# Kernel optimization log

Hardware: AMD Instinct MI355X
Metric: run time of the kernel (lower is better)

The kernel has to match this reference:

```python
import jax, jax.numpy as jnp
import numpy as np

NUM_HEADS = 16

def setup_inputs() -> dict:
    key = jax.random.key(0)
    ks = jax.random.split(key, 5)
    B, T, C = 2, 2048, 1024
    s = 0.02
    return {
        "x": jax.random.normal(ks[0], (B, T, C), dtype=jnp.float32),
        "in_w": jax.random.normal(ks[1], (3 * C, C), dtype=jnp.float32) * s,
        "in_b": jax.random.normal(ks[2], (3 * C,), dtype=jnp.float32) * s,
        "out_w": jax.random.normal(ks[3], (C, C), dtype=jnp.float32) * s,
        "out_b": jax.random.normal(ks[4], (C,), dtype=jnp.float32) * s,
    }

def reference(x, in_w, in_b, out_w, out_b):
    B, T, C = x.shape
    H = NUM_HEADS
    D = C // H
    qvk = x @ in_w.T + in_b  # (B, T, 3C)
    # einops 'b t (d k h) -> k b h t d': factor 3C as (D, 3, H), D outermost
    qvk = qvk.reshape(B, T, D, 3, H).transpose(3, 0, 4, 1, 2)  # (3, B, H, T, D)
    q, v, k = qvk[0], qvk[1], qvk[2]  # note q, v, k assignment order
    scores = jnp.einsum('bhid,bhjd->bhij', q, k) * (D ** -0.5)  # (B, H, T, T)
    causal = jnp.tril(jnp.ones((T, T), dtype=bool))
    scores = jnp.where(causal, scores, -jnp.inf)
    attn = jax.nn.softmax(scores, axis=-1)
    out = jnp.einsum('bhij,bhjd->bhid', attn, v)  # (B, H, T, D)
    out = out.transpose(0, 2, 1, 3).reshape(B, T, C)  # 'b h t d -> b t (h d)'
    return out @ out_w.T + out_b
```

## Files before the change

kernel.cpp:

```cpp
#include <hip/hip_runtime.h>


#define BB 2
#define TT 2048
#define CC 1024
#define HH 16
#define DD 64
#define MM (BB*TT)
#define N3 (3*CC)
#define BH (BB*HH)
#define KSCALE 0.18033688011112042f

typedef unsigned short u16;
typedef unsigned int   u32;
typedef __bf16 bf16x8 __attribute__((ext_vector_type(8)));
typedef float  f32x4  __attribute__((ext_vector_type(4)));

__device__ __forceinline__ u16 f32_to_bf16(float f) {
  u32 u = __float_as_uint(f);
  return (u16)((u + 0x7fffu + ((u >> 16) & 1u)) >> 16);
}
__device__ __forceinline__ u32 pack2_bf16(float a, float b) {
  u32 ua = __float_as_uint(a) + 0x8000u;
  u32 ub = __float_as_uint(b) + 0x8000u;
  return __builtin_amdgcn_perm(ub, ua, 0x07060302);
}

#define N4_X  (MM * CC / 4)
#define N4_W  (N3 * CC / 4)
#define N4_OW (CC * CC / 4)
__global__ __launch_bounds__(256) void cast_all(const float* __restrict__ x,
                                                const float* __restrict__ in_w,
                                                const float* __restrict__ out_w,
                                                u16* __restrict__ xb,
                                                u16* __restrict__ wb,
                                                u16* __restrict__ owb) {
  int i = blockIdx.x * 256 + threadIdx.x;
  const float* src; u16* dst; int j; int sj;
  if (i < N4_X)             { src = x;     dst = xb;  j = i;               sj = j; }
  else if (i < N4_X + N4_W) { src = in_w;  dst = wb;  j = i - N4_X;
                              int rp = j >> 8, c = j & 255;
                              int s = rp >> 10, h = (rp >> 6) & 15, d = rp & 63;
                              sj = (d * 48 + s * 16 + h) * 256 + c; }
  else                      { src = out_w; dst = owb; j = i - N4_X - N4_W; sj = j; }
  float4 f = reinterpret_cast<const float4*>(src)[sj];
  uint2 pk;
  pk.x = (u32)f32_to_bf16(f.x) | ((u32)f32_to_bf16(f.y) << 16);
  pk.y = (u32)f32_to_bf16(f.z) | ((u32)f32_to_bf16(f.w) << 16);
  reinterpret_cast<uint2*>(dst)[j] = pk;
}

__device__ __forceinline__ void gemm_core(const u16* __restrict__ Ag,
                                          const u16* __restrict__ Bg,
                                          int K, u16* Al, u16* Bl,
                                          int m0, int n0, f32x4 acc[4][4]) {
  const int tid = threadIdx.x, lane = tid & 63, w = tid >> 6;
  const int quad = lane >> 4, colr = lane & 15;
  const int mw = (w >> 1) * 64, nw = (w & 1) * 64;
  const int srow = lane >> 3, scol = lane & 7;
  const uint4* Al4 = reinterpret_cast<const uint4*>(Al);
  const uint4* Bl4 = reinterpret_cast<const uint4*>(Bl);
  for (int kt = 0; kt < K / 64; ++kt) {
    __syncthreads();
    #pragma unroll
    for (int ii = 0; ii < 4; ++ii) {
      int inst = w * 4 + ii;
      int row = inst * 8 + srow;
      int cs = scol ^ (row & 7);
      const u16* ga = Ag + (size_t)(m0 + row) * K + kt * 64 + cs * 8;
      const u16* gb = Bg + (size_t)(n0 + row) * K + kt * 64 + cs * 8;
      __builtin_amdgcn_global_load_lds(
          (const __attribute__((address_space(1))) void*)ga,
          (__attribute__((address_space(3))) void*)(Al + inst * 512), 16, 0, 0);
      __builtin_amdgcn_global_load_lds(
          (const __attribute__((address_space(1))) void*)gb,
          (__attribute__((address_space(3))) void*)(Bl + inst * 512), 16, 0, 0);
    }
    __syncthreads();
    #pragma unroll
    for (int ks = 0; ks < 2; ++ks) {
      bf16x8 af[4], bfr[4];
      #pragma unroll
      for (int t = 0; t < 4; ++t) {
        int mrow = mw + t * 16 + colr;
        af[t]  = __builtin_bit_cast(bf16x8, Al4[mrow * 8 + ((ks * 4 + quad) ^ (mrow & 7))]);
        int nrow = nw + t * 16 + colr;
        bfr[t] = __builtin_bit_cast(bf16x8, Bl4[nrow * 8 + ((ks * 4 + quad) ^ (nrow & 7))]);
      }
      #pragma unroll
      for (int mt = 0; mt < 4; ++mt)
        #pragma unroll
        for (int nt = 0; nt < 4; ++nt)
          acc[mt][nt] = __builtin_amdgcn_mfma_f32_16x16x32_bf16(af[mt], bfr[nt], acc[mt][nt], 0, 0, 0);
    }
  }
}

__global__ __launch_bounds__(256) void gemm_qkv(const u16* __restrict__ xb,
                                                const u16* __restrict__ wb,
                                                const float* __restrict__ in_b,
                                                u16* __restrict__ qkv) {
  __shared__ __align__(16) u16 Al[128 * 64];
  __shared__ __align__(16) u16 Bl[128 * 64];
  const int lane = threadIdx.x & 63, w = threadIdx.x >> 6;
  const int quad = lane >> 4, colr = lane & 15;
  const int mw = (w >> 1) * 64, nw = (w & 1) * 64;
  const int m0 = blockIdx.x * 128, n0 = blockIdx.y * 128;
  f32x4 acc[4][4];
  #pragma unroll
  for (int mt = 0; mt < 4; ++mt)
    #pragma unroll
    for (int nt = 0; nt < 4; ++nt) acc[mt][nt] = (f32x4){0.f, 0.f, 0.f, 0.f};
  gemm_core(xb, wb, CC, Al, Bl, m0, n0, acc);
  const int b_ = m0 >> 11;
  #pragma unroll
  for (int nt = 0; nt < 4; ++nt) {
    int np = n0 + nw + nt * 16 + colr;
    int s = np >> 10, h = (np >> 6) & 15, d = np & 63;
    float bias = in_b[d * 48 + s * 16 + h];
    float sc = (s == 2) ? KSCALE : 1.0f;
    u16* base = qkv + ((size_t)(s * BH + b_ * HH + h) * TT) * DD + d;
    #pragma unroll
    for (int mt = 0; mt < 4; ++mt)
      #pragma unroll
      for (int e = 0; e < 4; ++e) {
        int t = (m0 + mw + mt * 16 + quad * 4 + e) & (TT - 1);
        base[(size_t)t * DD] = f32_to_bf16((acc[mt][nt][e] + bias) * sc);
      }
  }
}

__global__ __launch_bounds__(128, 2) void attn_mfma(const u16* __restrict__ qkv,
                                                    u16* __restrict__ aout,
                                                    float* __restrict__ po,
                                                    float* __restrict__ pl) {
  __shared__ __align__(16) u32 Vt[2][64 * 36];
  __shared__ __align__(16) u32 Pl[2 * 32 * 36];
  const int tid  = threadIdx.x;
  const int lane = tid & 63, w = tid >> 6;
  const int quad = lane >> 4, colr = lane & 15;
  const int f = blockIdx.x;
  const int hf = (f >> 3) & 1;
  const int pr = (f >> 4) & 15;
  const int bh = (f & 7) * 4 + (f >> 8);
  const int b_ = bh >> 4, h = bh & 15;
  const int slot = (((bh << 4) + pr) << 1) | hf;

  const uint4* Qg4 = reinterpret_cast<const uint4*>(qkv + (size_t)bh * TT * DD);
  const uint4* Vg4 = reinterpret_cast<const uint4*>(qkv + ((size_t)BH + bh) * TT * DD);
  const uint4* Kg4 = reinterpret_cast<const uint4*>(qkv + ((size_t)2 * BH + bh) * TT * DD);
  const uint4* Pl4 = reinterpret_cast<const uint4*>(Pl);

  const int s_jp = tid & 31, s_half = tid >> 5;
  const int wb32 = w * (32 * 36);

  const int nseg = 2 - hf;
  for (int sg = 0; sg < nseg; ++sg) {
    const bool final_out = (hf == 0) && (sg == 0);
    const int qt  = final_out ? pr : (31 - pr);
    const int jlo = (hf == 1) ? (16 - pr) : 0;
    const int jhi = (hf == 1) ? (31 - pr) : (sg == 0 ? pr : 15 - pr);
    const int i0 = qt * 64;

    bf16x8 qa[2][2];
    #pragma unroll
    for (int u = 0; u < 2; ++u)
      #pragma unroll
      for (int ks = 0; ks < 2; ++ks)
        qa[u][ks] = __builtin_bit_cast(bf16x8,
            Qg4[(size_t)(i0 + w * 32 + u * 16 + colr) * 8 + ks * 4 + quad]);

    f32x4 oacc[2][4];
    #pragma unroll
    for (int u = 0; u < 2; ++u)
      #pragma unroll
      for (int dt = 0; dt < 4; ++dt) oacc[u][dt] = (f32x4){0.f, 0.f, 0.f, 0.f};
    float lp[2] = {0.f, 0.f};

    uint4 va[2], vb[2];
    #pragma unroll
    for (int io = 0; io < 2; ++io) {
      va[io] = Vg4[(size_t)(jlo * 64 + 2 * s_jp) * 8 + s_half + io * 4];
      vb[io] = Vg4[(size_t)(jlo * 64 + 2 * s_jp + 1) * 8 + s_half + io * 4];
    }

    for (int jt = jlo; jt <= jhi; ++jt) {
      const int j0 = jt * 64;
      u32* vtw = Vt[jt & 1];
      const uint4* vt4 = reinterpret_cast<const uint4*>(Vt[jt & 1]);

      #pragma unroll
      for (int io = 0; io < 2; ++io) {
        const int oc = s_half + io * 4;
        u32 aw[4] = {va[io].x, va[io].y, va[io].z, va[io].w};
        u32 bw[4] = {vb[io].x, vb[io].y, vb[io].z, vb[io].w};
        #pragma unroll
        for (int m = 0; m < 4; ++m) {
          vtw[(oc * 8 + 2 * m)     * 36 + s_jp] = __builtin_amdgcn_perm(bw[m], aw[m], 0x05040100);
          vtw[(oc * 8 + 2 * m + 1) * 36 + s_jp] = __builtin_amdgcn_perm(bw[m], aw[m], 0x07060302);
        }
      }
      if (jt < jhi) {
        int nj = j0 + 64;
        #pragma unroll
        for (int io = 0; io < 2; ++io) {
          va[io] = Vg4[(size_t)(nj + 2 * s_jp) * 8 + s_half + io * 4];
          vb[io] = Vg4[(size_t)(nj + 2 * s_jp + 1) * 8 + s_half + io * 4];
        }
      }
      __syncthreads();

      f32x4 sacc[2][4];
      #pragma unroll
      for (int u = 0; u < 2; ++u)
        #pragma unroll
        for (int t4 = 0; t4 < 4; ++t4) sacc[u][t4] = (f32x4){0.f, 0.f, 0.f, 0.f};
      #pragma unroll
      for (int ks = 0; ks < 2; ++ks) {
        uint4 kk[4];
        #pragma unroll
        for (int t4 = 0; t4 < 4; ++t4)
          kk[t4] = Kg4[(size_t)(j0 + t4 * 16 + colr) * 8 + ks * 4 + quad];
        #pragma unroll
        for (int t4 = 0; t4 < 4; ++t4) {
          bf16x8 kb = __builtin_bit_cast(bf16x8, kk[t4]);
          #pragma unroll
          for (int u = 0; u < 2; ++u)
            sacc[u][t4] = __builtin_amdgcn_mfma_f32_16x16x32_bf16(kb, qa[u][ks], sacc[u][t4], 0, 0, 0);
        }
      }

      if (jt == qt) {
        #pragma unroll
        for (int u = 0; u < 2; ++u) {
          const int qv = w * 32 + u * 16 + colr;
          #pragma unroll
          for (int t4 = 0; t4 < 4; ++t4) {
            float p0 = __builtin_amdgcn_exp2f(sacc[u][t4][0]);
            float p1 = __builtin_amdgcn_exp2f(sacc[u][t4][1]);
            float p2 = __builtin_amdgcn_exp2f(sacc[u][t4][2]);
            float p3 = __builtin_amdgcn_exp2f(sacc[u][t4][3]);
            int jb = t4 * 16 + quad * 4;
            if (jb + 0 > qv) p0 = 0.f;
            if (jb + 1 > qv) p1 = 0.f;
            if (jb + 2 > qv) p2 = 0.f;
            if (jb + 3 > qv) p3 = 0.f;
            lp[u] += (p0 + p1) + (p2 + p3);
            uint2 pw; pw.x = pack2_bf16(p0, p1); pw.y = pack2_bf16(p2, p3);
            *reinterpret_cast<uint2*>(Pl + wb32 + (u * 16 + colr) * 36 + t4 * 8 + quad * 2) = pw;
          }
        }
      } else {
        #pragma unroll
        for (int u = 0; u < 2; ++u)
          #pragma unroll
          for (int t4 = 0; t4 < 4; ++t4) {
            float p0 = __builtin_amdgcn_exp2f(sacc[u][t4][0]);
            float p1 = __builtin_amdgcn_exp2f(sacc[u][t4][1]);
            float p2 = __builtin_amdgcn_exp2f(sacc[u][t4][2]);
            float p3 = __builtin_amdgcn_exp2f(sacc[u][t4][3]);
            lp[u] += (p0 + p1) + (p2 + p3);
            uint2 pw; pw.x = pack2_bf16(p0, p1); pw.y = pack2_bf16(p2, p3);
            *reinterpret_cast<uint2*>(Pl + wb32 + (u * 16 + colr) * 36 + t4 * 8 + quad * 2) = pw;
          }
      }

      #pragma unroll
      for (int u = 0; u < 2; ++u) {
        bf16x8 pa[2];
        #pragma unroll
        for (int ks = 0; ks < 2; ++ks)
          pa[ks] = __builtin_bit_cast(bf16x8,
              Pl4[(wb32 + (u * 16 + colr) * 36 + ks * 16 + quad * 4) >> 2]);
        #pragma unroll
        for (int dt = 0; dt < 4; ++dt)
          #pragma unroll
          for (int ks = 0; ks < 2; ++ks) {
            bf16x8 vfr = __builtin_bit_cast(bf16x8, vt4[(dt * 16 + colr) * 9 + ks * 4 + quad]);
            oacc[u][dt] = __builtin_amdgcn_mfma_f32_16x16x32_bf16(pa[ks], vfr, oacc[u][dt], 0, 0, 0);
          }
      }
    }

    #pragma unroll
    for (int u = 0; u < 2; ++u) {
      float ls = lp[u];
      ls += __shfl_xor(ls, 16);
      ls += __shfl_xor(ls, 32);
      if (final_out) {
        float linv[4];
        #pragma unroll
        for (int rg = 0; rg < 4; ++rg)
          linv[rg] = 1.0f / __shfl(ls, quad * 4 + rg);
        #pragma unroll
        for (int dt = 0; dt < 4; ++dt)
          #pragma unroll
          for (int rg = 0; rg < 4; ++rg) {
            int ig = i0 + w * 32 + u * 16 + quad * 4 + rg;
            size_t off = ((size_t)(b_ * TT + ig)) * CC + h * DD + dt * 16 + colr;
            aout[off] = (u16)((__float_as_uint(oacc[u][dt][rg] * linv[rg]) + 0x8000u) >> 16);
          }
      } else {
        float* ob = po + (size_t)slot * 4096;
        #pragma unroll
        for (int dt = 0; dt < 4; ++dt)
          #pragma unroll
          for (int rg = 0; rg < 4; ++rg)
            ob[(w * 32 + u * 16 + quad * 4 + rg) * 64 + dt * 16 + colr] = oacc[u][dt][rg];
        if (quad == 0) pl[slot * 64 + w * 32 + u * 16 + colr] = ls;
      }
    }
    __syncthreads();
  }
}

__global__ __launch_bounds__(256) void attn_finalize(const float* __restrict__ po,
                                                     const float* __restrict__ pl,
                                                     u16* __restrict__ ab) {
  const int blk = blockIdx.x;
  const int bh = blk >> 4, pr = blk & 15;
  const int qt = 31 - pr;
  const int b_ = bh >> 4, h = bh & 15;
  const int t = threadIdx.x;
  const int r = t >> 2, dq = t & 3;
  const size_t s0 = (size_t)blk * 2, s1 = s0 + 1;
  const float4* o0 = reinterpret_cast<const float4*>(po + s0 * 4096 + r * 64 + dq * 16);
  const float4* o1 = reinterpret_cast<const float4*>(po + s1 * 4096 + r * 64 + dq * 16);
  float inv = 1.0f / (pl[s0 * 64 + r] + pl[s1 * 64 + r]);
  u16* dst = ab + ((size_t)(b_ * TT + qt * 64 + r)) * CC + h * DD + dq * 16;
  #pragma unroll
  for (int c = 0; c < 4; ++c) {
    float4 a = o0[c], b = o1[c];
    uint2 pk;
    pk.x = pack2_bf16((a.x + b.x) * inv, (a.y + b.y) * inv);
    pk.y = pack2_bf16((a.z + b.z) * inv, (a.w + b.w) * inv);
    *reinterpret_cast<uint2*>(dst + c * 4) = pk;
  }
}

__global__ __launch_bounds__(256) void gemm_out(const u16* __restrict__ ab,
                                                const u16* __restrict__ owb,
                                                const float* __restrict__ out_b,
                                                float* __restrict__ out) {
  __shared__ __align__(16) u16 Al[128 * 64];
  __shared__ __align__(16) u16 Bl[128 * 64];
  const int lane = threadIdx.x & 63, w = threadIdx.x >> 6;
  const int quad = lane >> 4, colr = lane & 15;
  const int mw = (w >> 1) * 64, nw = (w & 1) * 64;
  const int m0 = blockIdx.x * 128, n0 = blockIdx.y * 128;
  f32x4 acc[4][4];
  #pragma unroll
  for (int mt = 0; mt < 4; ++mt)
    #pragma unroll
    for (int nt = 0; nt < 4; ++nt) acc[mt][nt] = (f32x4){0.f, 0.f, 0.f, 0.f};
  gemm_core(ab, owb, CC, Al, Bl, m0, n0, acc);
  float bias[4];
  #pragma unroll
  for (int nt = 0; nt < 4; ++nt) bias[nt] = out_b[n0 + nw + nt * 16 + colr];
  #pragma unroll
  for (int mt = 0; mt < 4; ++mt)
    #pragma unroll
    for (int e = 0; e < 4; ++e) {
      int row = m0 + mw + mt * 16 + quad * 4 + e;
      #pragma unroll
      for (int nt = 0; nt < 4; ++nt)
        out[(size_t)row * CC + n0 + nw + nt * 16 + colr] = acc[mt][nt][e] + bias[nt];
    }
}

extern "C" void kernel_launch(void* const* d_in, const int* in_sizes, int n_in,
                              void* d_out, int out_size, void* d_ws, size_t ws_size,
                              hipStream_t stream) {
  const float* x     = (const float*)d_in[0];
  const float* in_w  = (const float*)d_in[1];
  const float* in_b  = (const float*)d_in[2];
  const float* out_w = (const float*)d_in[3];
  const float* out_b = (const float*)d_in[4];
  float* out = (float*)d_out;

  char* ws = (char*)d_ws;
  u16* xb   = (u16*)(ws + 0);
  u16* ab   = (u16*)(ws + 0);
  u16* wb   = (u16*)(ws + 8388608);
  u16* owb  = (u16*)(ws + 14680064);
  float* po = (float*)(ws + 16777216);
  float* pl = (float*)(ws + 16777216 + 16777216);
  u16* qkv  = (u16*)(ws + 41943040);

  cast_all<<<dim3((N4_X + N4_W + N4_OW) / 256), 256, 0, stream>>>(x, in_w, out_w, xb, wb, owb);

  gemm_qkv<<<dim3(MM / 128, N3 / 128), 256, 0, stream>>>(xb, wb, in_b, qkv);
  attn_mfma<<<dim3(1024), 128, 0, stream>>>(qkv, ab, po, pl);
  attn_finalize<<<dim3(512), 256, 0, stream>>>(po, pl, ab);
  gemm_out<<<dim3(MM / 128, CC / 128), 256, 0, stream>>>(ab, owb, out_b, out);
}
```

Before: 205.0 us.

## Software-pipeline QK^T scores one tile ahead and prefetch K into registers

K fragments for the next key tile are now prefetched into registers alongside the V prefetch. The QK^T MFMAs for tile jt+1 are issued after the softmax/P write of tile jt and before the PV MFMAs, so global K load latency is hidden and score MFMAs can overlap the exp and LDS work. The cost is higher register pressure from 8 extra uint4 K registers, and the score accumulators stay live across the loop, which may lower occupancy.

```diff
diff --git a/kernel.cpp b/kernel.cpp
--- a/kernel.cpp
+++ b/kernel.cpp
@@ -183,9 +183,29 @@
       va[io] = Vg4[(size_t)(jlo * 64 + 2 * s_jp) * 8 + s_half + io * 4];
       vb[io] = Vg4[(size_t)(jlo * 64 + 2 * s_jp + 1) * 8 + s_half + io * 4];
     }
+    uint4 kraw[8];
+    #pragma unroll
+    for (int t4 = 0; t4 < 4; ++t4)
+      #pragma unroll
+      for (int ks = 0; ks < 2; ++ks)
+        kraw[t4 * 2 + ks] = Kg4[(size_t)(jlo * 64 + t4 * 16 + colr) * 8 + ks * 4 + quad];
+
+    f32x4 sacc[2][4];
+    #pragma unroll
+    for (int u = 0; u < 2; ++u)
+      #pragma unroll
+      for (int t4 = 0; t4 < 4; ++t4) sacc[u][t4] = (f32x4){0.f, 0.f, 0.f, 0.f};
+    #pragma unroll
+    for (int ks = 0; ks < 2; ++ks)
+      #pragma unroll
+      for (int t4 = 0; t4 < 4; ++t4) {
+        bf16x8 kb = __builtin_bit_cast(bf16x8, kraw[t4 * 2 + ks]);
+        #pragma unroll
+        for (int u = 0; u < 2; ++u)
+          sacc[u][t4] = __builtin_amdgcn_mfma_f32_16x16x32_bf16(kb, qa[u][ks], sacc[u][t4], 0, 0, 0);
+      }
 
     for (int jt = jlo; jt <= jhi; ++jt) {
-      const int j0 = jt * 64;
       u32* vtw = Vt[jt & 1];
       const uint4* vt4 = reinterpret_cast<const uint4*>(Vt[jt & 1]);
 
@@ -201,34 +221,19 @@
         }
       }
       if (jt < jhi) {
-        int nj = j0 + 64;
+        const int nj = (jt + 1) * 64;
         #pragma unroll
         for (int io = 0; io < 2; ++io) {
           va[io] = Vg4[(size_t)(nj + 2 * s_jp) * 8 + s_half + io * 4];
           vb[io] = Vg4[(size_t)(nj + 2 * s_jp + 1) * 8 + s_half + io * 4];
         }
+        #pragma unroll
+        for (int t4 = 0; t4 < 4; ++t4)
+          #pragma unroll
+          for (int ks = 0; ks < 2; ++ks)
+            kraw[t4 * 2 + ks] = Kg4[(size_t)(nj + t4 * 16 + colr) * 8 + ks * 4 + quad];
       }
       __syncthreads();
-
-      f32x4 sacc[2][4];
-      #pragma unroll
-      for (int u = 0; u < 2; ++u)
-        #pragma unroll
-        for (int t4 = 0; t4 < 4; ++t4) sacc[u][t4] = (f32x4){0.f, 0.f, 0.f, 0.f};
-      #pragma unroll
-      for (int ks = 0; ks < 2; ++ks) {
-        uint4 kk[4];
-        #pragma unroll
-        for (int t4 = 0; t4 < 4; ++t4)
-          kk[t4] = Kg4[(size_t)(j0 + t4 * 16 + colr) * 8 + ks * 4 + quad];
-        #pragma unroll
-        for (int t4 = 0; t4 < 4; ++t4) {
-          bf16x8 kb = __builtin_bit_cast(bf16x8, kk[t4]);
-          #pragma unroll
-          for (int u = 0; u < 2; ++u)
-            sacc[u][t4] = __builtin_amdgcn_mfma_f32_16x16x32_bf16(kb, qa[u][ks], sacc[u][t4], 0, 0, 0);
-        }
-      }
 
       if (jt == qt) {
         #pragma unroll
@@ -265,6 +270,22 @@
           }
       }
 
+      if (jt < jhi) {
+        #pragma unroll
+        for (int u = 0; u < 2; ++u)
+          #pragma unroll
+          for (int t4 = 0; t4 < 4; ++t4) sacc[u][t4] = (f32x4){0.f, 0.f, 0.f, 0.f};
+        #pragma unroll
+        for (int ks = 0; ks < 2; ++ks)
+          #pragma unroll
+          for (int t4 = 0; t4 < 4; ++t4) {
+            bf16x8 kb = __builtin_bit_cast(bf16x8, kraw[t4 * 2 + ks]);
+            #pragma unroll
+            for (int u = 0; u < 2; ++u)
+              sacc[u][t4] = __builtin_amdgcn_mfma_f32_16x16x32_bf16(kb, qa[u][ks], sacc[u][t4], 0, 0, 0);
+          }
+      }
+
       #pragma unroll
       for (int u = 0; u < 2; ++u) {
         bf16x8 pa[2];
```

Measured after the change: 208.4 us. Within noise of the previous version (+1.7%).
